# Kernel tuning notes

Hardware: AMD Instinct MI355X
Metric: run time of the kernel (lower is better)

Reference implementation:

```python
import jax, jax.numpy as jnp
import numpy as np

N_NODES = 100000
N_EDGES = 1600000
IN_FEATS = 256
OUT_FEATS = 64


def setup_inputs() -> dict:
    key = jax.random.key(0)
    k1, k2, k3, k4, k5, k6 = jax.random.split(key, 6)
    x = jax.random.normal(k1, (N_NODES, IN_FEATS), dtype=jnp.float32)
    edge_src = jax.random.randint(k2, (N_EDGES,), 0, N_NODES, dtype=jnp.int32)
    edge_dst = jax.random.randint(k3, (N_EDGES,), 0, N_NODES, dtype=jnp.int32)
    edge_weight = jax.random.uniform(k4, (N_EDGES,), dtype=jnp.float32)
    # Linear(in_feats, out_feats) params (Kaiming-uniform-ish init scale)
    scale = 1.0 / np.sqrt(IN_FEATS)
    W = jax.random.uniform(k5, (IN_FEATS, OUT_FEATS), minval=-scale, maxval=scale, dtype=jnp.float32)
    b = jax.random.uniform(k6, (OUT_FEATS,), minval=-scale, maxval=scale, dtype=jnp.float32)
    return {"x": x, "edge_src": edge_src, "edge_dst": edge_dst,
            "edge_weight": edge_weight, "W": W, "b": b}


def reference(x, edge_src, edge_dst, edge_weight, W, b):
    # h = fc(x)
    h = x @ W + b                                   # [N, out_feats]
    # spmm(graph, h): out[dst] += w * h[src]  (weighted adjacency matvec)
    msgs = h[edge_src] * edge_weight[:, None]       # [E, out_feats]
    out = jax.ops.segment_sum(msgs, edge_dst, num_segments=N_NODES)
    return out
```

## Files before the change

kernel.cpp:

```cpp
#include <hip/hip_runtime.h>

#define IN_F 256
#define OUT_F 64
#define SORT_CHUNK 4096
#define BKT_SHIFT 7
#define BKT_NODES 128
#define MAX_NB 1024

typedef __attribute__((ext_vector_type(8))) short short8;
typedef __attribute__((ext_vector_type(4))) float f32x4;

static __device__ __forceinline__ short f2bf(float f) {
    union { float f; unsigned u; } v; v.f = f;
    unsigned r = v.u + 0x7FFFu + ((v.u >> 16) & 1u);
    return (short)(r >> 16);
}
static __device__ __forceinline__ float bf2f(short s) {
    return __int_as_float(((unsigned)(unsigned short)s) << 16);
}


static __device__ __forceinline__ void stage_W(const float* __restrict__ W,
                                               short* Wl, int tid) {
    const int n0 = tid & 63;
    const int kb = tid >> 6;
    #pragma unroll
    for (int K0 = 0; K0 < 64; K0 += 8) {
        const int k0 = kb * 64 + K0;
        short8 v;
        #pragma unroll
        for (int j = 0; j < 8; ++j)
            v[j] = f2bf(W[(k0 + j) * OUT_F + n0]);
        *(short8*)((char*)Wl + n0 * 512 + (((k0 >> 3)) ^ (n0 & 7)) * 16) = v;
    }
}

static __device__ __forceinline__ void gemm_tile(const float* __restrict__ x,
                                                 const short* Wl,
                                                 const float* __restrict__ bias,
                                                 short* __restrict__ h,
                                                 int rowbase, int nRows, int tid) {
    const int wv = tid >> 6;
    const int l  = tid & 63;
    const int lr = l & 15;
    const int kg = l >> 4;
    const int rb = rowbase + wv * 32;
    if (rb >= nRows) return;
    const int ar0 = min(rb + lr,      nRows - 1);
    const int ar1 = min(rb + 16 + lr, nRows - 1);
    const float* xp0 = x + (size_t)ar0 * IN_F + kg * 8;
    const float* xp1 = x + (size_t)ar1 * IN_F + kg * 8;

    f32x4 acc[2][4];
    #pragma unroll
    for (int m = 0; m < 2; ++m)
        #pragma unroll
        for (int n = 0; n < 4; ++n) acc[m][n] = (f32x4)0.f;

    #pragma unroll
    for (int kt = 0; kt < 8; ++kt) {
        const int K0 = kt * 32;
        float4 a0lo = *(const float4*)(xp0 + K0);
        float4 a0hi = *(const float4*)(xp0 + K0 + 4);
        float4 a1lo = *(const float4*)(xp1 + K0);
        float4 a1hi = *(const float4*)(xp1 + K0 + 4);

        short8 a0, a1;
        a0[0] = f2bf(a0lo.x); a0[1] = f2bf(a0lo.y);
        a0[2] = f2bf(a0lo.z); a0[3] = f2bf(a0lo.w);
        a0[4] = f2bf(a0hi.x); a0[5] = f2bf(a0hi.y);
        a0[6] = f2bf(a0hi.z); a0[7] = f2bf(a0hi.w);
        a1[0] = f2bf(a1lo.x); a1[1] = f2bf(a1lo.y);
        a1[2] = f2bf(a1lo.z); a1[3] = f2bf(a1lo.w);
        a1[4] = f2bf(a1hi.x); a1[5] = f2bf(a1hi.y);
        a1[6] = f2bf(a1hi.z); a1[7] = f2bf(a1hi.w);

        short8 bf[4];
        #pragma unroll
        for (int nt = 0; nt < 4; ++nt) {
            const int col = nt * 16 + lr;
            const int slot = (kt * 4 + kg) ^ (col & 7);
            bf[nt] = *(const short8*)((const char*)Wl + col * 512 + slot * 16);
        }
        #pragma unroll
        for (int nt = 0; nt < 4; ++nt) {
            acc[0][nt] = __builtin_amdgcn_mfma_f32_16x16x32_bf16(a0, bf[nt], acc[0][nt], 0, 0, 0);
            acc[1][nt] = __builtin_amdgcn_mfma_f32_16x16x32_bf16(a1, bf[nt], acc[1][nt], 0, 0, 0);
        }
    }

    #pragma unroll
    for (int m = 0; m < 2; ++m) {
        #pragma unroll
        for (int nt = 0; nt < 4; ++nt) {
            const int col = nt * 16 + lr;
            const float bb = bias[col];
            #pragma unroll
            for (int j = 0; j < 4; ++j) {
                const int r = rb + m * 16 + kg * 4 + j;
                if (r < nRows)
                    h[(size_t)r * OUT_F + col] = f2bf(acc[m][nt][j] + bb);
            }
        }
    }
}

static __device__ __forceinline__ void hist_chunk(const int* __restrict__ dst,
                                                  int* lh, int* __restrict__ counts,
                                                  int cb, int nE, int NB, int nSB,
                                                  int tid) {
    for (int b0 = tid; b0 < NB; b0 += 256) lh[b0] = 0;
    __syncthreads();
    const int base = cb * SORT_CHUNK;
    const int lim = min(nE, base + SORT_CHUNK);
    const int4* d4 = (const int4*)(dst + base);
    const int n4 = (lim - base) >> 2;
    for (int i = tid; i < n4; i += 256) {
        int4 v = d4[i];
        atomicAdd(&lh[v.x >> BKT_SHIFT], 1);
        atomicAdd(&lh[v.y >> BKT_SHIFT], 1);
        atomicAdd(&lh[v.z >> BKT_SHIFT], 1);
        atomicAdd(&lh[v.w >> BKT_SHIFT], 1);
    }
    for (int e = base + (n4 << 2) + tid; e < lim; e += 256)
        atomicAdd(&lh[dst[e] >> BKT_SHIFT], 1);
    __syncthreads();
    for (int b0 = tid; b0 < NB; b0 += 256)
        counts[b0 * nSB + cb] = lh[b0];
    __syncthreads();
}

static __device__ __forceinline__ void local_part_scan(
        const int* __restrict__ part, int nPart, int* partS, int* sh, int tid) {
    int v[4]; int sum = 0;
    #pragma unroll
    for (int i = 0; i < 4; ++i) {
        int idx = tid * 4 + i;
        v[i] = (idx < nPart) ? part[idx] : 0;
        sum += v[i];
    }
    sh[tid] = sum;
    __syncthreads();
    for (int d = 1; d < 256; d <<= 1) {
        int val = (tid >= d) ? sh[tid - d] : 0;
        __syncthreads();
        sh[tid] += val;
        __syncthreads();
    }
    int run = (tid == 0) ? 0 : sh[tid - 1];
    #pragma unroll
    for (int i = 0; i < 4; ++i) {
        partS[tid * 4 + i] = run;
        run += v[i];
    }
    __syncthreads();
}


__global__ __launch_bounds__(256, 4)
void fc_bhist_kernel(const float* __restrict__ x, const float* __restrict__ W,
                     const float* __restrict__ bias, short* __restrict__ h,
                     const int* __restrict__ dst, int* __restrict__ counts,
                     int nRows, int nE, int NB, int nSB, int nHist) {
    __shared__ __align__(16) char smem[32768];
    if ((int)blockIdx.x < nHist) {
        hist_chunk(dst, (int*)smem, counts, blockIdx.x, nE, NB, nSB, threadIdx.x);
        return;
    }
    short* Wl = (short*)smem;
    stage_W(W, Wl, threadIdx.x);
    __syncthreads();
    gemm_tile(x, Wl, bias, h, (blockIdx.x - nHist) * 128, nRows, threadIdx.x);
}

__global__ __launch_bounds__(256)
void scan1_kernel(const int* __restrict__ cnt, int* __restrict__ off,
                  int* __restrict__ part, int n) {
    __shared__ int sh[256];
    int base = blockIdx.x * 1024;
    int t = threadIdx.x;
    int v[4]; int s = 0;
    #pragma unroll
    for (int i = 0; i < 4; ++i) {
        int idx = base + t * 4 + i;
        v[i] = (idx < n) ? cnt[idx] : 0;
        s += v[i];
    }
    sh[t] = s;
    __syncthreads();
    for (int d = 1; d < 256; d <<= 1) {
        int val = (t >= d) ? sh[t - d] : 0;
        __syncthreads();
        sh[t] += val;
        __syncthreads();
    }
    if (t == 255) part[blockIdx.x] = sh[255];
    int run = (t == 0) ? 0 : sh[t - 1];
    #pragma unroll
    for (int i = 0; i < 4; ++i) {
        int idx = base + t * 4 + i;
        if (idx < n) off[idx] = run;
        run += v[i];
    }
}

__global__ __launch_bounds__(256)
void bfill_kernel(const int* __restrict__ src, const int* __restrict__ dst,
                  const float* __restrict__ w, const int* __restrict__ bases,
                  const int* __restrict__ part, int2* __restrict__ pack,
                  int nE, int NB, int nSB, int nPart) {
    __shared__ int cur[MAX_NB];
    __shared__ int partS[MAX_NB];
    __shared__ int sh[256];
    const int tid = threadIdx.x;
    const int cb = blockIdx.x;
    local_part_scan(part, nPart, partS, sh, tid);
    for (int b0 = tid; b0 < NB; b0 += 256) {
        int idx = b0 * nSB + cb;
        cur[b0] = bases[idx] + partS[idx >> 10];
    }
    __syncthreads();
    const int base = cb * SORT_CHUNK;
    const int lim = min(nE, base + SORT_CHUNK);
    const int4* s4 = (const int4*)(src + base);
    const int4* d4 = (const int4*)(dst + base);
    const float4* w4 = (const float4*)(w + base);
    const int n4 = (lim - base) >> 2;
    for (int i = tid; i < n4; i += 256) {
        int4 s = s4[i]; int4 d = d4[i]; float4 ww = w4[i];
        int p0 = atomicAdd(&cur[d.x >> BKT_SHIFT], 1);
        pack[p0] = make_int2(s.x | ((d.x & (BKT_NODES - 1)) << 17), __float_as_int(ww.x));
        int p1 = atomicAdd(&cur[d.y >> BKT_SHIFT], 1);
        pack[p1] = make_int2(s.y | ((d.y & (BKT_NODES - 1)) << 17), __float_as_int(ww.y));
        int p2 = atomicAdd(&cur[d.z >> BKT_SHIFT], 1);
        pack[p2] = make_int2(s.z | ((d.z & (BKT_NODES - 1)) << 17), __float_as_int(ww.z));
        int p3 = atomicAdd(&cur[d.w >> BKT_SHIFT], 1);
        pack[p3] = make_int2(s.w | ((d.w & (BKT_NODES - 1)) << 17), __float_as_int(ww.w));
    }
    for (int e = base + (n4 << 2) + tid; e < lim; e += 256) {
        int d = dst[e];
        int p = atomicAdd(&cur[d >> BKT_SHIFT], 1);
        pack[p] = make_int2(src[e] | ((d & (BKT_NODES - 1)) << 17),
                            __float_as_int(w[e]));
    }
}

__global__ __launch_bounds__(256)
void nsort_kernel(const int2* __restrict__ pack, const int* __restrict__ bases,
                  const int* __restrict__ part, int2* __restrict__ pack2,
                  int* __restrict__ off, int nRows, int nE, int NB, int nSB,
                  int nPart) {
    __shared__ int cnt[BKT_NODES];
    __shared__ int scn[BKT_NODES];
    __shared__ int partS[MAX_NB];
    __shared__ int sh[256];
    const int b = blockIdx.x;
    const int tid = threadIdx.x;
    local_part_scan(part, nPart, partS, sh, tid);

    const int i0 = b * nSB;
    const int segStart = bases[i0] + partS[i0 >> 10];
    int segEnd = nE;
    if (b + 1 < NB) {
        int i1 = (b + 1) * nSB;
        segEnd = bases[i1] + partS[i1 >> 10];
    }
    if (tid < BKT_NODES) cnt[tid] = 0;
    __syncthreads();
    {
        int e = segStart + tid;
        for (; e + 768 < segEnd; e += 1024) {
            int a0 = pack[e].x, a1 = pack[e + 256].x;
            int a2 = pack[e + 512].x, a3 = pack[e + 768].x;
            atomicAdd(&cnt[(a0 >> 17) & (BKT_NODES - 1)], 1);
            atomicAdd(&cnt[(a1 >> 17) & (BKT_NODES - 1)], 1);
            atomicAdd(&cnt[(a2 >> 17) & (BKT_NODES - 1)], 1);
            atomicAdd(&cnt[(a3 >> 17) & (BKT_NODES - 1)], 1);
        }
        for (; e < segEnd; e += 256)
            atomicAdd(&cnt[(pack[e].x >> 17) & (BKT_NODES - 1)], 1);
    }
    __syncthreads();
    if (tid < BKT_NODES) scn[tid] = cnt[tid];
    __syncthreads();
    for (int d = 1; d < BKT_NODES; d <<= 1) {
        int t = 0;
        if (tid < BKT_NODES && tid >= d) t = scn[tid - d];
        __syncthreads();
        if (tid < BKT_NODES) scn[tid] += t;
        __syncthreads();
    }
    const int node0 = b * BKT_NODES;
    const int ncnt = min(BKT_NODES, nRows - node0);
    if (tid < ncnt)
        off[node0 + tid] = segStart + scn[tid] - cnt[tid];
    if (tid == 0 && node0 + ncnt == nRows)
        off[nRows] = segEnd;
    __syncthreads();
    if (tid < BKT_NODES) cnt[tid] = segStart + scn[tid] - cnt[tid];
    __syncthreads();
    {
        int e = segStart + tid;
        for (; e + 768 < segEnd; e += 1024) {
            int2 p0 = pack[e], p1 = pack[e + 256];
            int2 p2 = pack[e + 512], p3 = pack[e + 768];
            int q0 = atomicAdd(&cnt[(p0.x >> 17) & (BKT_NODES - 1)], 1);
            pack2[q0] = make_int2(p0.x & 0x1FFFF, p0.y);
            int q1 = atomicAdd(&cnt[(p1.x >> 17) & (BKT_NODES - 1)], 1);
            pack2[q1] = make_int2(p1.x & 0x1FFFF, p1.y);
            int q2 = atomicAdd(&cnt[(p2.x >> 17) & (BKT_NODES - 1)], 1);
            pack2[q2] = make_int2(p2.x & 0x1FFFF, p2.y);
            int q3 = atomicAdd(&cnt[(p3.x >> 17) & (BKT_NODES - 1)], 1);
            pack2[q3] = make_int2(p3.x & 0x1FFFF, p3.y);
        }
        for (; e < segEnd; e += 256) {
            int2 p = pack[e];
            int q = atomicAdd(&cnt[(p.x >> 17) & (BKT_NODES - 1)], 1);
            pack2[q] = make_int2(p.x & 0x1FFFF, p.y);
        }
    }
}

__global__ __launch_bounds__(256)
void ngather_kernel(const short* __restrict__ h, const int* __restrict__ off,
                    const int2* __restrict__ pack2, float* __restrict__ out,
                    int nNodes) {
    int wid = (blockIdx.x * 256 + threadIdx.x) >> 6;
    int lane = threadIdx.x & 63;
    if (wid >= nNodes) return;
    int e = off[wid], end = off[wid + 1];
    const ushort* hu = (const ushort*)h;
    float acc = 0.f;
    for (; e + 8 <= end; e += 8) {
        int2 pk[8];
        #pragma unroll
        for (int i = 0; i < 8; ++i) pk[i] = pack2[e + i];
        float hv[8];
        #pragma unroll
        for (int i = 0; i < 8; ++i)
            hv[i] = bf2f((short)hu[(size_t)pk[i].x * OUT_F + lane]);
        #pragma unroll
        for (int i = 0; i < 8; ++i)
            acc = fmaf(__int_as_float(pk[i].y), hv[i], acc);
    }
    for (; e + 4 <= end; e += 4) {
        int2 pk[4];
        #pragma unroll
        for (int i = 0; i < 4; ++i) pk[i] = pack2[e + i];
        #pragma unroll
        for (int i = 0; i < 4; ++i)
            acc = fmaf(__int_as_float(pk[i].y),
                       bf2f((short)hu[(size_t)pk[i].x * OUT_F + lane]), acc);
    }
    for (; e < end; ++e) {
        int2 p = pack2[e];
        acc = fmaf(__int_as_float(p.y),
                   bf2f((short)hu[(size_t)p.x * OUT_F + lane]), acc);
    }
    out[(size_t)wid * OUT_F + lane] = acc;
}

__global__ __launch_bounds__(256)
void scatter_kernel(const short* __restrict__ h, const int* __restrict__ src,
                    const int* __restrict__ dst, const float* __restrict__ w,
                    float* __restrict__ out, int nE) {
    int t = blockIdx.x * 256 + threadIdx.x;
    int c = t & 15;
    int stride = (gridDim.x * 256) >> 4;
    for (int e = t >> 4; e < nE; e += stride) {
        int s = src[e];
        int d = dst[e];
        float ww = w[e];
        float* op = out + (size_t)d * OUT_F + c * 4;
        const short* hp = h + (size_t)s * OUT_F + c * 4;
        unsafeAtomicAdd(op + 0, ww * bf2f(hp[0]));
        unsafeAtomicAdd(op + 1, ww * bf2f(hp[1]));
        unsafeAtomicAdd(op + 2, ww * bf2f(hp[2]));
        unsafeAtomicAdd(op + 3, ww * bf2f(hp[3]));
    }
}

static inline size_t align256(size_t x) { return (x + 255) & ~(size_t)255; }

extern "C" void kernel_launch(void* const* d_in, const int* in_sizes, int n_in,
                              void* d_out, int out_size, void* d_ws, size_t ws_size,
                              hipStream_t stream) {
    const float* x    = (const float*)d_in[0];
    const int*   esrc = (const int*)d_in[1];
    const int*   edst = (const int*)d_in[2];
    const float* ew   = (const float*)d_in[3];
    const float* W    = (const float*)d_in[4];
    const float* b    = (const float*)d_in[5];

    int nRows = in_sizes[0] / IN_F;
    int nE    = in_sizes[1];

    int NB  = (nRows + BKT_NODES - 1) / BKT_NODES;
    int nSB = (nE + SORT_CHUNK - 1) / SORT_CHUNK;
    int nCnt = NB * nSB;
    int nPart = (nCnt + 1023) / 1024;

    char* p = (char*)d_ws;
    size_t hB    = align256((size_t)nRows * OUT_F * sizeof(short));
    size_t cntB  = align256((size_t)nCnt * sizeof(int));
    size_t basB  = align256((size_t)nCnt * sizeof(int));
    size_t partB = align256((size_t)nPart * sizeof(int));
    size_t packB = align256((size_t)nE * sizeof(int2));
    size_t offB  = align256((size_t)(nRows + 1) * sizeof(int));
    size_t need  = hB + cntB + basB + partB + 2 * packB + offB;

    short* h      = (short*)p;  p += hB;
    int*   counts = (int*)p;    p += cntB;
    int*   bases  = (int*)p;    p += basB;
    int*   part   = (int*)p;    p += partB;
    int2*  pack   = (int2*)p;   p += packB;
    int2*  pack2  = (int2*)p;   p += packB;
    int*   off    = (int*)p;

    float* out = (float*)d_out;

    bool ok = (ws_size >= need) && (NB <= MAX_NB) && (nPart <= 1024) &&
              (nRows < (1 << 17));
    int fcBlocks = (nRows + 127) / 128;

    if (!ok) {
        fc_bhist_kernel<<<fcBlocks, 256, 0, stream>>>(
            x, W, b, h, edst, counts, nRows, nE, NB, nSB, 0);
        hipMemsetAsync(out, 0, (size_t)out_size * sizeof(float), stream);
        scatter_kernel<<<4096, 256, 0, stream>>>(h, esrc, edst, ew, out, nE);
        return;
    }

    fc_bhist_kernel<<<nSB + fcBlocks, 256, 0, stream>>>(
        x, W, b, h, edst, counts, nRows, nE, NB, nSB, nSB);
    scan1_kernel<<<nPart, 256, 0, stream>>>(counts, bases, part, nCnt);
    bfill_kernel<<<nSB, 256, 0, stream>>>(esrc, edst, ew, bases, part,
                                          pack, nE, NB, nSB, nPart);
    nsort_kernel<<<NB, 256, 0, stream>>>(pack, bases, part, pack2, off,
                                         nRows, nE, NB, nSB, nPart);
    int gBlocks = (nRows * 64 + 255) / 256;
    ngather_kernel<<<gBlocks, 256, 0, stream>>>(h, off, pack2, out, nRows);
}
```

Before: 284.7 us.

## Pre-convert W to bf16 once, process two GEMM tiles per block, widen gather unroll

A small prep kernel converts W to a transposed bf16 copy once, so each GEMM block stages W into LDS with vectorized 16-byte copies instead of strided fp32 loads and per-element conversion. Each GEMM block now processes two 128-row tiles, which halves the number of W staging passes. The gather loop gets a 16-edge unrolled stage to put more independent loads in flight. The cost is one extra kernel launch, fewer GEMM blocks in flight (less parallelism) and higher register pressure in the gather.

```diff
diff --git a/kernel.cpp b/kernel.cpp
--- a/kernel.cpp
+++ b/kernel.cpp
@@ -20,18 +20,14 @@
 }
 
 
-static __device__ __forceinline__ void stage_W(const float* __restrict__ W,
-                                               short* Wl, int tid) {
-    const int n0 = tid & 63;
-    const int kb = tid >> 6;
-    #pragma unroll
-    for (int K0 = 0; K0 < 64; K0 += 8) {
-        const int k0 = kb * 64 + K0;
-        short8 v;
-        #pragma unroll
-        for (int j = 0; j < 8; ++j)
-            v[j] = f2bf(W[(k0 + j) * OUT_F + n0]);
-        *(short8*)((char*)Wl + n0 * 512 + (((k0 >> 3)) ^ (n0 & 7)) * 16) = v;
+static __device__ __forceinline__ void stage_Wt(const short* __restrict__ Wt,
+                                                short* Wl, int tid) {
+    const uint4* src = (const uint4*)Wt;
+    #pragma unroll
+    for (int it = 0; it < 8; ++it) {
+        int g = it * 256 + tid;
+        int n = g >> 5, s = g & 31;
+        *(uint4*)((char*)Wl + n * 512 + (s ^ (n & 7)) * 16) = src[g];
     }
 }
 
@@ -157,8 +153,17 @@
 }
 
 
+__global__ __launch_bounds__(256)
+void prep_w_kernel(const float* __restrict__ W, short* __restrict__ Wt) {
+    int i = blockIdx.x * 256 + threadIdx.x;
+    if (i < IN_F * OUT_F) {
+        int k = i / OUT_F, n = i % OUT_F;
+        Wt[n * IN_F + k] = f2bf(W[i]);
+    }
+}
+
 __global__ __launch_bounds__(256, 4)
-void fc_bhist_kernel(const float* __restrict__ x, const float* __restrict__ W,
+void fc_bhist_kernel(const float* __restrict__ x, const short* __restrict__ Wt,
                      const float* __restrict__ bias, short* __restrict__ h,
                      const int* __restrict__ dst, int* __restrict__ counts,
                      int nRows, int nE, int NB, int nSB, int nHist) {
@@ -168,9 +173,11 @@
         return;
     }
     short* Wl = (short*)smem;
-    stage_W(W, Wl, threadIdx.x);
-    __syncthreads();
-    gemm_tile(x, Wl, bias, h, (blockIdx.x - nHist) * 128, nRows, threadIdx.x);
+    stage_Wt(Wt, Wl, threadIdx.x);
+    __syncthreads();
+    const int fb = blockIdx.x - nHist;
+    gemm_tile(x, Wl, bias, h, (fb * 2 + 0) * 128, nRows, threadIdx.x);
+    gemm_tile(x, Wl, bias, h, (fb * 2 + 1) * 128, nRows, threadIdx.x);
 }
 
 __global__ __launch_bounds__(256)
@@ -331,6 +338,18 @@
     int e = off[wid], end = off[wid + 1];
     const ushort* hu = (const ushort*)h;
     float acc = 0.f;
+    for (; e + 16 <= end; e += 16) {
+        int2 pk[16];
+        #pragma unroll
+        for (int i = 0; i < 16; ++i) pk[i] = pack2[e + i];
+        float hv[16];
+        #pragma unroll
+        for (int i = 0; i < 16; ++i)
+            hv[i] = bf2f((short)hu[(size_t)pk[i].x * OUT_F + lane]);
+        #pragma unroll
+        for (int i = 0; i < 16; ++i)
+            acc = fmaf(__int_as_float(pk[i].y), hv[i], acc);
+    }
     for (; e + 8 <= end; e += 8) {
         int2 pk[8];
         #pragma unroll
@@ -402,14 +421,16 @@
 
     char* p = (char*)d_ws;
     size_t hB    = align256((size_t)nRows * OUT_F * sizeof(short));
+    size_t wtB   = align256((size_t)IN_F * OUT_F * sizeof(short));
     size_t cntB  = align256((size_t)nCnt * sizeof(int));
     size_t basB  = align256((size_t)nCnt * sizeof(int));
     size_t partB = align256((size_t)nPart * sizeof(int));
     size_t packB = align256((size_t)nE * sizeof(int2));
     size_t offB  = align256((size_t)(nRows + 1) * sizeof(int));
-    size_t need  = hB + cntB + basB + partB + 2 * packB + offB;
+    size_t need  = hB + wtB + cntB + basB + partB + 2 * packB + offB;
 
     short* h      = (short*)p;  p += hB;
+    short* Wt     = (short*)p;  p += wtB;
     int*   counts = (int*)p;    p += cntB;
     int*   bases  = (int*)p;    p += basB;
     int*   part   = (int*)p;    p += partB;
@@ -421,18 +442,20 @@
 
     bool ok = (ws_size >= need) && (NB <= MAX_NB) && (nPart <= 1024) &&
               (nRows < (1 << 17));
-    int fcBlocks = (nRows + 127) / 128;
+    int nGemm = (nRows + 255) / 256;
+
+    prep_w_kernel<<<(IN_F * OUT_F + 255) / 256, 256, 0, stream>>>(W, Wt);
 
     if (!ok) {
-        fc_bhist_kernel<<<fcBlocks, 256, 0, stream>>>(
-            x, W, b, h, edst, counts, nRows, nE, NB, nSB, 0);
+        fc_bhist_kernel<<<nGemm, 256, 0, stream>>>(
+            x, Wt, b, h, edst, counts, nRows, nE, NB, nSB, 0);
         hipMemsetAsync(out, 0, (size_t)out_size * sizeof(float), stream);
         scatter_kernel<<<4096, 256, 0, stream>>>(h, esrc, edst, ew, out, nE);
         return;
     }
 
-    fc_bhist_kernel<<<nSB + fcBlocks, 256, 0, stream>>>(
-        x, W, b, h, edst, counts, nRows, nE, NB, nSB, nSB);
+    fc_bhist_kernel<<<nSB + nGemm, 256, 0, stream>>>(
+        x, Wt, b, h, edst, counts, nRows, nE, NB, nSB, nSB);
     scan1_kernel<<<nPart, 256, 0, stream>>>(counts, bases, part, nCnt);
     bfill_kernel<<<nSB, 256, 0, stream>>>(esrc, edst, ew, bases, part,
                                           pack, nE, NB, nSB, nPart);
```

Result: no change. 289.7 us (+1.8%).
